# Performance work log

Hardware: AMD Instinct MI355X
Metric: run time of the kernel (lower is better)

## Reference

```python
import jax, jax.numpy as jnp
import numpy as np

N = 50000      # nodes
E = 800000     # edges
F_IN = 128     # n_features
H = 4          # n_heads
C1 = 64        # n_hidden (per-head out of layer 1)
C2 = 32        # n_classes (per-head out of layer 2)
NEG_SLOPE = 0.2
EPS = 1e-16


def setup_inputs() -> dict:
    key = jax.random.key(0)
    ks = jax.random.split(key, 12)
    x = jax.random.normal(ks[0], (N, F_IN), dtype=jnp.float32)
    edge_index = jax.random.randint(ks[1], (2, E), 0, N, dtype=jnp.int64)
    # layer 1 params (GATConv: shared lin for src/dst, att_src/att_dst vectors, bias)
    W1 = jax.random.normal(ks[2], (F_IN, H * C1), dtype=jnp.float32) * (1.0 / np.sqrt(F_IN))
    att_src1 = jax.random.normal(ks[3], (H, C1), dtype=jnp.float32) * 0.1
    att_dst1 = jax.random.normal(ks[4], (H, C1), dtype=jnp.float32) * 0.1
    b1 = jnp.zeros((C1,), dtype=jnp.float32)
    # layer 2 params
    W2 = jax.random.normal(ks[5], (C1, H * C2), dtype=jnp.float32) * (1.0 / np.sqrt(C1))
    att_src2 = jax.random.normal(ks[6], (H, C2), dtype=jnp.float32) * 0.1
    att_dst2 = jax.random.normal(ks[7], (H, C2), dtype=jnp.float32) * 0.1
    b2 = jnp.zeros((C2,), dtype=jnp.float32)
    return {"x": x, "edge_index": edge_index,
            "W1": W1, "att_src1": att_src1, "att_dst1": att_dst1, "b1": b1,
            "W2": W2, "att_src2": att_src2, "att_dst2": att_dst2, "b2": b2}


def gat_conv(x, src, dst, W, att_src, att_dst, b, heads, out_ch):
    """PyG GATConv with concat=False (head-averaged output)."""
    n = x.shape[0]
    h = (x @ W).reshape(n, heads, out_ch)                 # [N, H, C]
    a_s = jnp.einsum('nhc,hc->nh', h, att_src)            # [N, H]
    a_d = jnp.einsum('nhc,hc->nh', h, att_dst)            # [N, H]
    e = jax.nn.leaky_relu(a_s[src] + a_d[dst], NEG_SLOPE)  # [E, H]
    # segment softmax over edges grouped by destination node
    m = jax.ops.segment_max(e, dst, num_segments=n)        # [N, H]
    m = jnp.where(jnp.isfinite(m), m, 0.0)
    ex = jnp.exp(e - m[dst])                               # [E, H]
    denom = jax.ops.segment_sum(ex, dst, num_segments=n)   # [N, H]
    alpha = ex / (denom[dst] + EPS)                        # [E, H]
    # scatter-add aggregation of attended source features
    msg = alpha[:, :, None] * h[src]                       # [E, H, C]
    out = jax.ops.segment_sum(msg, dst, num_segments=n)    # [N, H, C]
    return out.mean(axis=1) + b                            # [N, C]


def reference(x, edge_index, W1, att_src1, att_dst1, b1, W2, att_src2, att_dst2, b2):
    src, dst = edge_index[0], edge_index[1]
    h = jax.nn.relu(gat_conv(x, src, dst, W1, att_src1, att_dst1, b1, H, C1))
    # dropout is identity in eval mode
    out = gat_conv(h, src, dst, W2, att_src2, att_dst2, b2, H, C2)
    return out
```

## Files before the change

### kernel.cpp

```cpp
#include <hip/hip_runtime.h>
#include <hip/hip_fp16.h>
#include <cstdint>
#include <cstddef>

#define N_NODES 50000
#define N_EDGES 800000
#define F_IN 128
#define H_HEADS 4
#define C1 64
#define C2 32
#define NEG_SLOPE 0.2f
#define EPS_GAT 1e-16f
#define SLOT_CAP 96
#define FILL_BPG 256
#define NODES_PER_GROUP 6250

typedef _Float16 half8 __attribute__((ext_vector_type(8)));
typedef float f32x4 __attribute__((ext_vector_type(4)));

template<int K, int M>
__device__ __forceinline__ void wtrans_dev(const float* __restrict__ W,
                                           _Float16* __restrict__ Wt,
                                           _Float16* tile, int bm, int bk) {
    const int m0 = bm * 64, k0 = bk * 64;
    const int t = threadIdx.x;
    const int c = t & 63;
#pragma unroll
    for (int j = 0; j < 16; ++j) {
        int r = (t >> 6) + 4 * j;
        tile[c * 66 + r] = (_Float16)W[(size_t)(k0 + r) * M + m0 + c];
    }
    __syncthreads();
#pragma unroll
    for (int j = 0; j < 16; ++j) {
        int m_l = (t >> 6) + 4 * j;
        Wt[(size_t)(m0 + m_l) * K + k0 + c] = tile[m_l * 66 + c];
    }
}

__global__ __launch_bounds__(256) void fill_wtrans_kernel(
        const int* __restrict__ src, const int* __restrict__ dst,
        int* __restrict__ cursor, unsigned short* __restrict__ slots,
        const float* __restrict__ W1, _Float16* __restrict__ wt1,
        const float* __restrict__ W2, _Float16* __restrict__ wt2) {
    __shared__ _Float16 tile[64 * 66];
    const int b = blockIdx.x;
    if (b < 8) {
        wtrans_dev<F_IN, H_HEADS * C1>(W1, wt1, tile, b & 3, b >> 2);
    } else if (b < 10) {
        wtrans_dev<C1, H_HEADS * C2>(W2, wt2, tile, b - 8, 0);
    }
    const int g = b & 7;
    const int bg = b >> 3;
    const int dlo = g * NODES_PER_GROUP;
    const int dhi = dlo + NODES_PER_GROUP;
    for (int e = bg * 256 + (int)threadIdx.x; e < N_EDGES; e += FILL_BPG * 256) {
        int d = dst[e];
        if (d >= dlo && d < dhi) {
            int p = atomicAdd(&cursor[d], 1);
            if (p < SLOT_CAP) slots[(size_t)d * SLOT_CAP + p] = (unsigned short)src[e];
        }
    }
}

template<int K, int M, int Hn, int C, typename InT>
__global__ __launch_bounds__(256) void gemm_att_kernel(
        const InT* __restrict__ X, const _Float16* __restrict__ Wt,
        _Float16* __restrict__ Hout,
        const float* __restrict__ atts, const float* __restrict__ attd,
        float* __restrict__ as_, float* __restrict__ ad_, int Nr) {
    constexpr int LDK = K + 8;
    constexpr int NCT = M / 64;
    constexpr int HPB = 64 / C;
    __shared__ _Float16 Ah[64 * LDK];
    __shared__ _Float16 Bt[64 * LDK];
    __shared__ _Float16 Ht[64 * 72];
    const int row0 = blockIdx.x * 64;
    const int t = threadIdx.x;
    const int wv = t >> 6;
    const int lane = t & 63;
    const int quad = lane >> 4;
    const int n16 = lane & 15;

    if constexpr (sizeof(InT) == 4) {
        constexpr int KQ = K / 4;
#pragma unroll
        for (int j = 0; j < (64 * KQ) / 256; ++j) {
            int flat = t + 256 * j;
            int r = flat / KQ, kq = flat % KQ;
            int rg = row0 + r;
            float4 v = make_float4(0.f, 0.f, 0.f, 0.f);
            if (rg < Nr) v = *(const float4*)&X[(size_t)rg * K + 4 * kq];
            _Float16 tmp[4] = {(_Float16)v.x, (_Float16)v.y, (_Float16)v.z, (_Float16)v.w};
            *(uint2*)&Ah[r * LDK + 4 * kq] = *(const uint2*)tmp;
        }
    } else {
        constexpr int KQ = K / 8;
#pragma unroll
        for (int j = 0; j < (64 * KQ) / 256; ++j) {
            int flat = t + 256 * j;
            int r = flat / KQ, kq = flat % KQ;
            int rg = row0 + r;
            uint4 v = make_uint4(0u, 0u, 0u, 0u);
            if (rg < Nr) v = *(const uint4*)&X[(size_t)rg * K + 8 * kq];
            *(uint4*)&Ah[r * LDK + 8 * kq] = v;
        }
    }
    __syncthreads();

    half8 af[K / 32];
    const _Float16* Ap = &Ah[(16 * wv + n16) * LDK + 8 * quad];
#pragma unroll
    for (int ki = 0; ki < K / 32; ++ki) af[ki] = *(const half8*)(Ap + 32 * ki);

    for (int ct = 0; ct < NCT; ++ct) {
        const int col0 = 64 * ct;
        __syncthreads();
        {
            constexpr int KQ8 = K / 8;
#pragma unroll
            for (int j = 0; j < (64 * KQ8) / 256; ++j) {
                int flat = t + 256 * j;
                int c = flat / KQ8, kq = flat % KQ8;
                uint4 v = *(const uint4*)&Wt[(size_t)(col0 + c) * K + 8 * kq];
                *(uint4*)&Bt[c * LDK + 8 * kq] = v;
            }
        }
        __syncthreads();

        f32x4 acc[4];
#pragma unroll
        for (int nf = 0; nf < 4; ++nf) acc[nf] = (f32x4){0.f, 0.f, 0.f, 0.f};
#pragma unroll
        for (int ki = 0; ki < K / 32; ++ki) {
#pragma unroll
            for (int nf = 0; nf < 4; ++nf) {
                half8 bf = *(const half8*)&Bt[(16 * nf + n16) * LDK + 32 * ki + 8 * quad];
                acc[nf] = __builtin_amdgcn_mfma_f32_16x16x32_f16(af[ki], bf, acc[nf], 0, 0, 0);
            }
        }

        float dps[HPB][4], dpd[HPB][4];
#pragma unroll
        for (int u = 0; u < HPB; ++u)
#pragma unroll
            for (int r = 0; r < 4; ++r) { dps[u][r] = 0.f; dpd[u][r] = 0.f; }
#pragma unroll
        for (int nf = 0; nf < 4; ++nf) {
            int gc = col0 + 16 * nf + n16;
            float cs = atts[gc], cd = attd[gc];
#pragma unroll
            for (int r = 0; r < 4; ++r) {
                float av = acc[nf][r];
                dps[(16 * nf) / C][r] += av * cs;
                dpd[(16 * nf) / C][r] += av * cd;
            }
        }
#pragma unroll
        for (int u = 0; u < HPB; ++u)
#pragma unroll
            for (int r = 0; r < 4; ++r) {
                float s = dps[u][r], d = dpd[u][r];
#pragma unroll
                for (int off = 1; off < 16; off <<= 1) {
                    s += __shfl_xor(s, off, 64);
                    d += __shfl_xor(d, off, 64);
                }
                dps[u][r] = s; dpd[u][r] = d;
            }
        if (n16 == 0) {
            const int h0 = col0 / C;
#pragma unroll
            for (int r = 0; r < 4; ++r) {
                int row = row0 + 16 * wv + 4 * quad + r;
                if (row < Nr) {
#pragma unroll
                    for (int u = 0; u < HPB; ++u) {
                        as_[row * Hn + h0 + u] = dps[u][r];
                        ad_[row * Hn + h0 + u] = dpd[u][r];
                    }
                }
            }
        }

#pragma unroll
        for (int nf = 0; nf < 4; ++nf)
#pragma unroll
            for (int r = 0; r < 4; ++r)
                Ht[(16 * wv + 4 * quad + r) * 72 + 16 * nf + n16] = (_Float16)acc[nf][r];
        __syncthreads();
#pragma unroll
        for (int j = 0; j < 2; ++j) {
            int chunk = t + 256 * j;
            int r = chunk >> 3, cc = chunk & 7;
            int row = row0 + r;
            if (row < Nr) {
                uint4 v = *(const uint4*)&Ht[r * 72 + 8 * cc];
                *(uint4*)&Hout[(size_t)row * M + col0 + 8 * cc] = v;
            }
        }
    }
}

template<int Hn, int C, bool RELU, bool OUT_F16>
__global__ __launch_bounds__(256) void gat_agg_kernel(
        const int* __restrict__ degp, const unsigned short* __restrict__ slots,
        const float* __restrict__ as_, const float* __restrict__ ad_,
        const _Float16* __restrict__ Hm, const float* __restrict__ bias,
        void* __restrict__ outv, int Nr) {
    constexpr int HC = Hn * C;
    constexpr int PER = HC / 16;
    constexpr int NV = PER / 8;
    int node = blockIdx.x * 4 + (threadIdx.x >> 6);
    int lane = threadIdx.x & 63;
    if (node >= Nr) return;
    const int g = lane >> 4;
    const int l = lane & 15;
    const int h = l >> 2;
    const float ad_h = ad_[node * Hn + h];

    const int dn = min(degp[node], SLOT_CAP);
    const int begin = node * SLOT_CAP;
    const int end = begin + dn;
    const int iters = (dn + 3) >> 2;

    float acc[PER];
#pragma unroll
    for (int t = 0; t < PER; ++t) acc[t] = 0.f;
    float wsum = 0.f;

    int idx = begin + g;
    int s_cur = (idx < end) ? (int)slots[idx] : -1;
    int s_nx = (idx + 4 < end) ? (int)slots[idx + 4] : -1;
    float a_cur = 0.f;
    uint4 u_cur[NV] = {};
    if (s_cur >= 0) {
        a_cur = as_[s_cur * Hn + h];
        const uint4* hp = (const uint4*)(Hm + (size_t)s_cur * HC + l * PER);
        u_cur[0] = hp[0];
        if constexpr (NV == 2) u_cur[1] = hp[1];
    }

    for (int it = 0; it < iters; ++it) {
        const int s_pf = s_nx;
        s_nx = (idx + 8 < end) ? (int)slots[idx + 8] : -1;
        float a_nx = 0.f;
        uint4 u_nx[NV] = {};
        if (s_pf >= 0) {
            a_nx = as_[s_pf * Hn + h];
            const uint4* hp = (const uint4*)(Hm + (size_t)s_pf * HC + l * PER);
            u_nx[0] = hp[0];
            if constexpr (NV == 2) u_nx[1] = hp[1];
        }
        float logit = a_cur + ad_h;
        logit = (logit > 0.f) ? logit : NEG_SLOPE * logit;
        float w = (s_cur >= 0) ? __expf(logit) : 0.f;
        wsum += w;
#pragma unroll
        for (int v = 0; v < NV; ++v) {
            float2 f;
            f = __half22float2(*(const __half2*)&u_cur[v].x);
            acc[8 * v + 0] += w * f.x; acc[8 * v + 1] += w * f.y;
            f = __half22float2(*(const __half2*)&u_cur[v].y);
            acc[8 * v + 2] += w * f.x; acc[8 * v + 3] += w * f.y;
            f = __half22float2(*(const __half2*)&u_cur[v].z);
            acc[8 * v + 4] += w * f.x; acc[8 * v + 5] += w * f.y;
            f = __half22float2(*(const __half2*)&u_cur[v].w);
            acc[8 * v + 6] += w * f.x; acc[8 * v + 7] += w * f.y;
        }
        s_cur = s_pf; a_cur = a_nx;
#pragma unroll
        for (int v = 0; v < NV; ++v) u_cur[v] = u_nx[v];
        idx += 4;
    }

#pragma unroll
    for (int t = 0; t < PER; ++t) {
        acc[t] += __shfl_xor(acc[t], 16, 64);
        acc[t] += __shfl_xor(acc[t], 32, 64);
    }
    wsum += __shfl_xor(wsum, 16, 64);
    wsum += __shfl_xor(wsum, 32, 64);
    const float inv = 1.f / (wsum + EPS_GAT);
    float val[PER];
#pragma unroll
    for (int t = 0; t < PER; ++t) {
        float v = acc[t] * inv;
        v += __shfl_xor(v, 4, 64);
        v += __shfl_xor(v, 8, 64);
        val[t] = v * (1.0f / Hn);
    }
    if (lane < 4) {
        const int c0 = lane * PER;
#pragma unroll
        for (int t = 0; t < PER; ++t) {
            float v = val[t] + bias[c0 + t];
            if (RELU) v = fmaxf(v, 0.f);
            val[t] = v;
        }
        if constexpr (OUT_F16) {
            _Float16* o = (_Float16*)outv;
            _Float16 tmp[PER];
#pragma unroll
            for (int t = 0; t < PER; ++t) tmp[t] = (_Float16)val[t];
            uint4* d4 = (uint4*)&o[(size_t)node * C + c0];
            d4[0] = *(const uint4*)&tmp[0];
            if constexpr (NV == 2) d4[1] = *(const uint4*)&tmp[8];
        } else {
            float* o = (float*)outv;
#pragma unroll
            for (int t4 = 0; t4 < PER / 4; ++t4)
                *(float4*)&o[(size_t)node * C + c0 + 4 * t4] =
                    make_float4(val[4 * t4 + 0], val[4 * t4 + 1],
                                val[4 * t4 + 2], val[4 * t4 + 3]);
        }
    }
}

extern "C" void kernel_launch(void* const* d_in, const int* in_sizes, int n_in,
                              void* d_out, int out_size, void* d_ws, size_t ws_size,
                              hipStream_t stream) {
    const float* x    = (const float*)d_in[0];
    const int*   ei   = (const int*)d_in[1];
    const float* W1   = (const float*)d_in[2];
    const float* as1w = (const float*)d_in[3];
    const float* ad1w = (const float*)d_in[4];
    const float* b1   = (const float*)d_in[5];
    const float* W2   = (const float*)d_in[6];
    const float* as2w = (const float*)d_in[7];
    const float* ad2w = (const float*)d_in[8];
    const float* b2   = (const float*)d_in[9];
    float* out = (float*)d_out;

    const int* src = ei;
    const int* dst = ei + N_EDGES;

    char* ws = (char*)d_ws;
    size_t off = 0;
    auto alloc = [&](size_t bytes) -> void* {
        void* p = ws + off;
        off = (off + bytes + 255) & ~(size_t)255;
        return p;
    };
    int*   cursor = (int*)alloc((size_t)N_NODES * 4);
    float* as1_ = (float*)alloc((size_t)N_NODES * H_HEADS * 4);
    float* ad1_ = (float*)alloc((size_t)N_NODES * H_HEADS * 4);
    float* as2_ = (float*)alloc((size_t)N_NODES * H_HEADS * 4);
    float* ad2_ = (float*)alloc((size_t)N_NODES * H_HEADS * 4);
    _Float16* h1   = (_Float16*)alloc((size_t)N_NODES * H_HEADS * C1 * 2);
    _Float16* out1 = (_Float16*)alloc((size_t)N_NODES * C1 * 2);
    _Float16* h2   = (_Float16*)alloc((size_t)N_NODES * H_HEADS * C2 * 2);
    _Float16* wt1  = (_Float16*)alloc((size_t)(H_HEADS * C1) * F_IN * 2);
    _Float16* wt2  = (_Float16*)alloc((size_t)(H_HEADS * C2) * C1 * 2);
    unsigned short* slots = (unsigned short*)alloc((size_t)N_NODES * SLOT_CAP * 2);

    hipMemsetAsync(cursor, 0, (size_t)N_NODES * 4, stream);

    fill_wtrans_kernel<<<8 * FILL_BPG, 256, 0, stream>>>(
        src, dst, cursor, slots, W1, wt1, W2, wt2);

    gemm_att_kernel<F_IN, H_HEADS * C1, H_HEADS, C1, float>
        <<<(N_NODES + 63) / 64, 256, 0, stream>>>(
            x, wt1, h1, as1w, ad1w, as1_, ad1_, N_NODES);

    gat_agg_kernel<H_HEADS, C1, true, true><<<(N_NODES + 3) / 4, 256, 0, stream>>>(
        cursor, slots, as1_, ad1_, h1, b1, (void*)out1, N_NODES);

    gemm_att_kernel<C1, H_HEADS * C2, H_HEADS, C2, _Float16>
        <<<(N_NODES + 63) / 64, 256, 0, stream>>>(
            out1, wt2, h2, as2w, ad2w, as2_, ad2_, N_NODES);

    gat_agg_kernel<H_HEADS, C2, false, false><<<(N_NODES + 3) / 4, 256, 0, stream>>>(
        cursor, slots, as2_, ad2_, h2, b2, (void*)out, N_NODES);
}
```

Before: 252.5 us.

## Fuse layer-2 linear projection and attention logits into layer-1 aggregation kernel

The layer-1 aggregation kernel now also computes the layer-2 projection. Each block converts W2 to fp16 pairs in shared memory, and each wave multiplies its node's 64-wide activated output by W2 through shuffles, then writes h2 and the layer-2 attention scalars directly. This removes the out1 round trip through global memory and one kernel launch. In exchange, every block reloads and converts the 32 KB W2, and every wave does about 64 shuffles per node. Separately, the edge-fill loop reads src/dst as int4 vectors to cut load instruction count.

```diff
diff --git a/kernel.cpp b/kernel.cpp
--- a/kernel.cpp
+++ b/kernel.cpp
@@ -41,24 +41,37 @@
 __global__ __launch_bounds__(256) void fill_wtrans_kernel(
         const int* __restrict__ src, const int* __restrict__ dst,
         int* __restrict__ cursor, unsigned short* __restrict__ slots,
-        const float* __restrict__ W1, _Float16* __restrict__ wt1,
-        const float* __restrict__ W2, _Float16* __restrict__ wt2) {
+        const float* __restrict__ W1, _Float16* __restrict__ wt1) {
     __shared__ _Float16 tile[64 * 66];
     const int b = blockIdx.x;
     if (b < 8) {
         wtrans_dev<F_IN, H_HEADS * C1>(W1, wt1, tile, b & 3, b >> 2);
-    } else if (b < 10) {
-        wtrans_dev<C1, H_HEADS * C2>(W2, wt2, tile, b - 8, 0);
     }
     const int g = b & 7;
     const int bg = b >> 3;
     const int dlo = g * NODES_PER_GROUP;
     const int dhi = dlo + NODES_PER_GROUP;
-    for (int e = bg * 256 + (int)threadIdx.x; e < N_EDGES; e += FILL_BPG * 256) {
-        int d = dst[e];
-        if (d >= dlo && d < dhi) {
-            int p = atomicAdd(&cursor[d], 1);
-            if (p < SLOT_CAP) slots[(size_t)d * SLOT_CAP + p] = (unsigned short)src[e];
+    const int4* dst4 = (const int4*)dst;
+    const int4* src4 = (const int4*)src;
+    constexpr int NV4 = N_EDGES / 4;
+    for (int v = bg * 256 + (int)threadIdx.x; v < NV4; v += FILL_BPG * 256) {
+        int4 d4 = dst4[v];
+        int4 s4 = src4[v];
+        if (d4.x >= dlo && d4.x < dhi) {
+            int p = atomicAdd(&cursor[d4.x], 1);
+            if (p < SLOT_CAP) slots[(size_t)d4.x * SLOT_CAP + p] = (unsigned short)s4.x;
+        }
+        if (d4.y >= dlo && d4.y < dhi) {
+            int p = atomicAdd(&cursor[d4.y], 1);
+            if (p < SLOT_CAP) slots[(size_t)d4.y * SLOT_CAP + p] = (unsigned short)s4.y;
+        }
+        if (d4.z >= dlo && d4.z < dhi) {
+            int p = atomicAdd(&cursor[d4.z], 1);
+            if (p < SLOT_CAP) slots[(size_t)d4.z * SLOT_CAP + p] = (unsigned short)s4.z;
+        }
+        if (d4.w >= dlo && d4.w < dhi) {
+            int p = atomicAdd(&cursor[d4.w], 1);
+            if (p < SLOT_CAP) slots[(size_t)d4.w * SLOT_CAP + p] = (unsigned short)s4.w;
         }
     }
 }
@@ -202,15 +215,32 @@
     }
 }
 
-template<int Hn, int C, bool RELU, bool OUT_F16>
+template<int Hn, int C, bool RELU, bool OUT_F16, bool FUSE2>
 __global__ __launch_bounds__(256) void gat_agg_kernel(
         const int* __restrict__ degp, const unsigned short* __restrict__ slots,
         const float* __restrict__ as_, const float* __restrict__ ad_,
         const _Float16* __restrict__ Hm, const float* __restrict__ bias,
-        void* __restrict__ outv, int Nr) {
+        void* __restrict__ outv, int Nr,
+        const float* __restrict__ W2raw, const float* __restrict__ atts2,
+        const float* __restrict__ attd2,
+        float* __restrict__ as2o, float* __restrict__ ad2o,
+        _Float16* __restrict__ h2o) {
     constexpr int HC = Hn * C;
     constexpr int PER = HC / 16;
     constexpr int NV = PER / 8;
+    __shared__ unsigned int wt2p[FUSE2 ? 64 * 64 : 1];
+
+    if constexpr (FUSE2) {
+#pragma unroll
+        for (int it = 0; it < 16; ++it) {
+            int idx = (int)threadIdx.x + 256 * it;
+            float2 v = ((const float2*)W2raw)[idx];
+            _Float16 p[2] = {(_Float16)v.x, (_Float16)v.y};
+            wt2p[idx] = *(const unsigned int*)p;
+        }
+        __syncthreads();
+    }
+
     int node = blockIdx.x * 4 + (threadIdx.x >> 6);
     int lane = threadIdx.x & 63;
     if (node >= Nr) return;
@@ -290,29 +320,62 @@
         v += __shfl_xor(v, 8, 64);
         val[t] = v * (1.0f / Hn);
     }
-    if (lane < 4) {
-        const int c0 = lane * PER;
-#pragma unroll
-        for (int t = 0; t < PER; ++t) {
-            float v = val[t] + bias[c0 + t];
-            if (RELU) v = fmaxf(v, 0.f);
-            val[t] = v;
-        }
-        if constexpr (OUT_F16) {
-            _Float16* o = (_Float16*)outv;
-            _Float16 tmp[PER];
-#pragma unroll
-            for (int t = 0; t < PER; ++t) tmp[t] = (_Float16)val[t];
-            uint4* d4 = (uint4*)&o[(size_t)node * C + c0];
-            d4[0] = *(const uint4*)&tmp[0];
-            if constexpr (NV == 2) d4[1] = *(const uint4*)&tmp[8];
-        } else {
-            float* o = (float*)outv;
-#pragma unroll
-            for (int t4 = 0; t4 < PER / 4; ++t4)
-                *(float4*)&o[(size_t)node * C + c0 + 4 * t4] =
-                    make_float4(val[4 * t4 + 0], val[4 * t4 + 1],
-                                val[4 * t4 + 2], val[4 * t4 + 3]);
+    const int cq = (lane & 3) * PER;
+#pragma unroll
+    for (int t = 0; t < PER; ++t) {
+        float v = val[t] + bias[cq + t];
+        if (RELU) v = fmaxf(v, 0.f);
+        val[t] = v;
+    }
+
+    if constexpr (FUSE2) {
+        float h2a = 0.f, h2b = 0.f;
+#pragma unroll
+        for (int q = 0; q < 4; ++q) {
+#pragma unroll
+            for (int t = 0; t < 16; ++t) {
+                float yk = __shfl(val[t], q, 64);
+                unsigned int wp = wt2p[(q * 16 + t) * 64 + lane];
+                float2 f = __half22float2(*(const __half2*)&wp);
+                h2a += yk * f.x;
+                h2b += yk * f.y;
+            }
+        }
+        _Float16 hh[2] = {(_Float16)h2a, (_Float16)h2b};
+        *(unsigned int*)&h2o[(size_t)node * 128 + 2 * lane] = *(const unsigned int*)hh;
+        float2 a2 = *(const float2*)&atts2[2 * lane];
+        float2 d2 = *(const float2*)&attd2[2 * lane];
+        float ps = h2a * a2.x + h2b * a2.y;
+        float pd = h2a * d2.x + h2b * d2.y;
+#pragma unroll
+        for (int off = 1; off < 16; off <<= 1) {
+            ps += __shfl_xor(ps, off, 64);
+            pd += __shfl_xor(pd, off, 64);
+        }
+        if ((lane & 15) == 0) {
+            int h2h = lane >> 4;
+            as2o[node * Hn + h2h] = ps;
+            ad2o[node * Hn + h2h] = pd;
+        }
+    } else {
+        if (lane < 4) {
+            const int c0 = lane * PER;
+            if constexpr (OUT_F16) {
+                _Float16* o = (_Float16*)outv;
+                _Float16 tmp[PER];
+#pragma unroll
+                for (int t = 0; t < PER; ++t) tmp[t] = (_Float16)val[t];
+                uint4* d4 = (uint4*)&o[(size_t)node * C + c0];
+                d4[0] = *(const uint4*)&tmp[0];
+                if constexpr (NV == 2) d4[1] = *(const uint4*)&tmp[8];
+            } else {
+                float* o = (float*)outv;
+#pragma unroll
+                for (int t4 = 0; t4 < PER / 4; ++t4)
+                    *(float4*)&o[(size_t)node * C + c0 + 4 * t4] =
+                        make_float4(val[4 * t4 + 0], val[4 * t4 + 1],
+                                    val[4 * t4 + 2], val[4 * t4 + 3]);
+            }
         }
     }
 }
@@ -348,28 +411,24 @@
     float* as2_ = (float*)alloc((size_t)N_NODES * H_HEADS * 4);
     float* ad2_ = (float*)alloc((size_t)N_NODES * H_HEADS * 4);
     _Float16* h1   = (_Float16*)alloc((size_t)N_NODES * H_HEADS * C1 * 2);
-    _Float16* out1 = (_Float16*)alloc((size_t)N_NODES * C1 * 2);
     _Float16* h2   = (_Float16*)alloc((size_t)N_NODES * H_HEADS * C2 * 2);
     _Float16* wt1  = (_Float16*)alloc((size_t)(H_HEADS * C1) * F_IN * 2);
-    _Float16* wt2  = (_Float16*)alloc((size_t)(H_HEADS * C2) * C1 * 2);
     unsigned short* slots = (unsigned short*)alloc((size_t)N_NODES * SLOT_CAP * 2);
 
     hipMemsetAsync(cursor, 0, (size_t)N_NODES * 4, stream);
 
     fill_wtrans_kernel<<<8 * FILL_BPG, 256, 0, stream>>>(
-        src, dst, cursor, slots, W1, wt1, W2, wt2);
+        src, dst, cursor, slots, W1, wt1);
 
     gemm_att_kernel<F_IN, H_HEADS * C1, H_HEADS, C1, float>
         <<<(N_NODES + 63) / 64, 256, 0, stream>>>(
             x, wt1, h1, as1w, ad1w, as1_, ad1_, N_NODES);
 
-    gat_agg_kernel<H_HEADS, C1, true, true><<<(N_NODES + 3) / 4, 256, 0, stream>>>(
-        cursor, slots, as1_, ad1_, h1, b1, (void*)out1, N_NODES);
-
-    gemm_att_kernel<C1, H_HEADS * C2, H_HEADS, C2, _Float16>
-        <<<(N_NODES + 63) / 64, 256, 0, stream>>>(
-            out1, wt2, h2, as2w, ad2w, as2_, ad2_, N_NODES);
-
-    gat_agg_kernel<H_HEADS, C2, false, false><<<(N_NODES + 3) / 4, 256, 0, stream>>>(
-        cursor, slots, as2_, ad2_, h2, b2, (void*)out, N_NODES);
+    gat_agg_kernel<H_HEADS, C1, true, true, true><<<(N_NODES + 3) / 4, 256, 0, stream>>>(
+        cursor, slots, as1_, ad1_, h1, b1, nullptr, N_NODES,
+        W2, as2w, ad2w, as2_, ad2_, h2);
+
+    gat_agg_kernel<H_HEADS, C2, false, false, false><<<(N_NODES + 3) / 4, 256, 0, stream>>>(
+        cursor, slots, as2_, ad2_, h2, b2, (void*)out, N_NODES,
+        nullptr, nullptr, nullptr, nullptr, nullptr, nullptr);
 }
```

Result: slower. 285.2 us (+13.0%).
